# Optimization experiments

Measured on AMD Instinct MI355X. Metric: run time of the kernel, lower is better.

The kernel has to match this reference:

```python
import jax, jax.numpy as jnp
import numpy as np

H = 1024
V_IN = 32000
V_OUT = 32000
L = 256
START_ID = 1


def _gru_cell(x, h, Wi, Wh, bi, bh):
    # PyTorch GRU cell. x,h: [H]; Wi,Wh: [3H,H]; bi,bh: [3H]
    gi = Wi @ x + bi
    gh = Wh @ h + bh
    ir, iz, inn = jnp.split(gi, 3)
    hr, hz, hn = jnp.split(gh, 3)
    r = jax.nn.sigmoid(ir + hr)
    z = jax.nn.sigmoid(iz + hz)
    n = jnp.tanh(inn + r * hn)
    return (1.0 - z) * n + z * h


def setup_inputs() -> dict:
    key = jax.random.key(0)
    ks = jax.random.split(key, 20)
    s = 0.02
    d = {
        "input_ids": jax.random.randint(ks[0], (L,), 0, V_IN),
        "target_ids": jax.random.randint(ks[1], (L,), 0, V_OUT),
        "enc_emb": jax.random.normal(ks[2], (V_IN, H), jnp.float32) * s,
        "enc_Wi": jax.random.normal(ks[3], (3 * H, H), jnp.float32) * s,
        "enc_Wh": jax.random.normal(ks[4], (3 * H, H), jnp.float32) * s,
        "enc_bi": jnp.zeros((3 * H,), jnp.float32),
        "enc_bh": jnp.zeros((3 * H,), jnp.float32),
        "dec_emb": jax.random.normal(ks[5], (V_OUT, H), jnp.float32) * s,
        "dec_Wi": jax.random.normal(ks[6], (3 * H, H), jnp.float32) * s,
        "dec_Wh": jax.random.normal(ks[7], (3 * H, H), jnp.float32) * s,
        "dec_bi": jnp.zeros((3 * H,), jnp.float32),
        "dec_bh": jnp.zeros((3 * H,), jnp.float32),
        "attn_W": jax.random.normal(ks[8], (L, 2 * H), jnp.float32) * s,
        "attn_b": jnp.zeros((L,), jnp.float32),
        "comb_W": jax.random.normal(ks[9], (H, 2 * H), jnp.float32) * s,
        "comb_b": jnp.zeros((H,), jnp.float32),
        "out_W": jax.random.normal(ks[10], (V_OUT, H), jnp.float32) * s,
        "out_b": jnp.zeros((V_OUT,), jnp.float32),
    }
    return d


def reference(input_ids, target_ids, enc_emb, enc_Wi, enc_Wh, enc_bi, enc_bh,
              dec_emb, dec_Wi, dec_Wh, dec_bi, dec_bh,
              attn_W, attn_b, comb_W, comb_b, out_W, out_b):
    # ---- encoder: per-step GRU over input tokens, batch=1 ----
    enc_x = enc_emb[input_ids]  # [L, H]

    def enc_step(h, x):
        h2 = _gru_cell(x, h, enc_Wi, enc_Wh, enc_bi, enc_bh)
        return h2, h2

    h0 = jnp.zeros((H,), enc_emb.dtype)
    enc_hidden, enc_outs = jax.lax.scan(enc_step, h0, enc_x)  # enc_outs: [L, H]

    # ---- decoder with teacher forcing (deterministic branch) ----
    dec_in_ids = jnp.concatenate([jnp.array([START_ID], input_ids.dtype), target_ids[:-1]])

    def dec_step(h, inp):
        tok, tgt = inp
        e = dec_emb[tok]  # [H] (dropout in eval mode = identity)
        scores = attn_W @ jnp.concatenate([e, h]) + attn_b  # [L]
        a = jax.nn.softmax(scores)
        ctx = a @ enc_outs  # [H]
        c = jax.nn.relu(comb_W @ jnp.concatenate([e, ctx]) + comb_b)
        h2 = _gru_cell(c, h, dec_Wi, dec_Wh, dec_bi, dec_bh)
        logp = jax.nn.log_softmax(out_W @ h2 + out_b)  # [V_OUT]
        return h2, -logp[tgt]

    _, nll = jax.lax.scan(dec_step, enc_hidden, (dec_in_ids, target_ids))
    return jnp.sum(nll)
```

## Files before the change

kernel.cpp:

```cpp
#include <hip/hip_runtime.h>
#include <math.h>

#define H 1024
#define SEQ 256
#define VOUT 32000

typedef unsigned long long u64;

__device__ __forceinline__ float sigmoidf_(float x) { return 1.f / (1.f + expf(-x)); }

__device__ __forceinline__ u64 aload64(const u64* p) {
    return __hip_atomic_load(p, __ATOMIC_RELAXED, __HIP_MEMORY_SCOPE_AGENT);
}
__device__ __forceinline__ void publish(u64* p, float v, unsigned tag) {
    u64 pk = ((u64)tag << 32) | (u64)__float_as_uint(v);
    __hip_atomic_store(p, pk, __ATOMIC_RELAXED, __HIP_MEMORY_SCOPE_AGENT);
}
__device__ __forceinline__ float wait1(const u64* p, unsigned tag) {
    u64 v = aload64(p);
    while ((unsigned)(v >> 32) != tag) {
        __builtin_amdgcn_s_sleep(1);
        v = aload64(p);
    }
    return __uint_as_float((unsigned)v);
}
__device__ __forceinline__ void wait4(const u64* p0, const u64* p1,
                                      const u64* p2, const u64* p3, unsigned tag,
                                      float& o0, float& o1, float& o2, float& o3) {
    u64 v0 = aload64(p0), v1 = aload64(p1), v2 = aload64(p2), v3 = aload64(p3);
    while ((unsigned)(v0 >> 32) != tag || (unsigned)(v1 >> 32) != tag ||
           (unsigned)(v2 >> 32) != tag || (unsigned)(v3 >> 32) != tag) {
        __builtin_amdgcn_s_sleep(1);
        v0 = aload64(p0); v1 = aload64(p1); v2 = aload64(p2); v3 = aload64(p3);
    }
    o0 = __uint_as_float((unsigned)v0);
    o1 = __uint_as_float((unsigned)v1);
    o2 = __uint_as_float((unsigned)v2);
    o3 = __uint_as_float((unsigned)v3);
}

__global__ __launch_bounds__(256) void gather_kernel(
    const int* __restrict__ input_ids, const int* __restrict__ target_ids,
    const float* __restrict__ enc_emb, const float* __restrict__ dec_emb,
    float* __restrict__ enc_x, float* __restrict__ dec_e)
{
    int b = blockIdx.x, tid = threadIdx.x;
    if (b < SEQ) {
        int tok = input_ids[b];
        const float4* src = (const float4*)(enc_emb + (size_t)tok * H);
        float4* dst = (float4*)(enc_x + (size_t)b * H);
        dst[tid] = src[tid];
    } else {
        int t = b - SEQ;
        int tok = (t == 0) ? 1 : target_ids[t - 1];
        const float4* src = (const float4*)(dec_emb + (size_t)tok * H);
        float4* dst = (float4*)(dec_e + (size_t)t * H);
        dst[tid] = src[tid];
    }
}

__global__ __launch_bounds__(256) void init_kernel(u64* __restrict__ h64)
{
    int i = blockIdx.x * 256 + threadIdx.x;
    if (i < 2 * H) h64[i] = 0ULL;
}

__global__ __launch_bounds__(256) void gemm_nt_kernel(
    const float* __restrict__ A, const float* __restrict__ B,
    const float* __restrict__ bias, float* __restrict__ C,
    int Kdim, int lda, int offa, int ldb, int ldc)
{
    __shared__ float As[16][68];
    __shared__ float Bs[16][68];
    const int tid = threadIdx.x;
    const int m0 = blockIdx.y * 64;
    const int n0 = blockIdx.x * 64;
    const int tr = (tid >> 4) << 2;
    const int tc = (tid & 15) << 2;
    const int lrow = tid >> 2;
    const int lk = (tid & 3) << 2;
    const float* Ab = A + (size_t)m0 * lda + offa;
    const float* Bb = B + (size_t)n0 * ldb;
    float acc[4][4] = {{0.f,0.f,0.f,0.f},{0.f,0.f,0.f,0.f},{0.f,0.f,0.f,0.f},{0.f,0.f,0.f,0.f}};

    for (int k0 = 0; k0 < Kdim; k0 += 16) {
        float4 av = *(const float4*)(Ab + (size_t)lrow * lda + (k0 + lk));
        float4 bv = *(const float4*)(Bb + (size_t)lrow * ldb + (k0 + lk));
        As[lk + 0][lrow] = av.x; As[lk + 1][lrow] = av.y;
        As[lk + 2][lrow] = av.z; As[lk + 3][lrow] = av.w;
        Bs[lk + 0][lrow] = bv.x; Bs[lk + 1][lrow] = bv.y;
        Bs[lk + 2][lrow] = bv.z; Bs[lk + 3][lrow] = bv.w;
        __syncthreads();
#pragma unroll
        for (int k = 0; k < 16; ++k) {
            float4 a = *(const float4*)(&As[k][tr]);
            float4 b = *(const float4*)(&Bs[k][tc]);
            acc[0][0] = fmaf(a.x, b.x, acc[0][0]);
            acc[0][1] = fmaf(a.x, b.y, acc[0][1]);
            acc[0][2] = fmaf(a.x, b.z, acc[0][2]);
            acc[0][3] = fmaf(a.x, b.w, acc[0][3]);
            acc[1][0] = fmaf(a.y, b.x, acc[1][0]);
            acc[1][1] = fmaf(a.y, b.y, acc[1][1]);
            acc[1][2] = fmaf(a.y, b.z, acc[1][2]);
            acc[1][3] = fmaf(a.y, b.w, acc[1][3]);
            acc[2][0] = fmaf(a.z, b.x, acc[2][0]);
            acc[2][1] = fmaf(a.z, b.y, acc[2][1]);
            acc[2][2] = fmaf(a.z, b.z, acc[2][2]);
            acc[2][3] = fmaf(a.z, b.w, acc[2][3]);
            acc[3][0] = fmaf(a.w, b.x, acc[3][0]);
            acc[3][1] = fmaf(a.w, b.y, acc[3][1]);
            acc[3][2] = fmaf(a.w, b.z, acc[3][2]);
            acc[3][3] = fmaf(a.w, b.w, acc[3][3]);
        }
        __syncthreads();
    }
#pragma unroll
    for (int i = 0; i < 4; ++i) {
#pragma unroll
        for (int j = 0; j < 4; ++j) {
            float v = acc[i][j];
            if (bias) v += bias[n0 + tc + j];
            C[(size_t)(m0 + tr + i) * ldc + (n0 + tc + j)] = v;
        }
    }
}

__global__ __launch_bounds__(256, 1) void enc_rnn_kernel(
    const float* __restrict__ Wh, const float* __restrict__ bh,
    const float* __restrict__ gi_all,
    u64* __restrict__ h64, float* __restrict__ encH)
{
    __shared__ float h_s[2][H];
    const int tid = threadIdx.x;
    const int wave = tid >> 6, lane = tid & 63;
    const int u = blockIdx.x * 4 + wave;

    float rWr[16], rWz[16], rWn[16];
    {
        const float* wr = Wh + (size_t)u * H;
        const float* wz = Wh + (size_t)(u + H) * H;
        const float* wn = Wh + (size_t)(u + 2 * H) * H;
#pragma unroll
        for (int i = 0; i < 16; ++i) {
            int k = lane + (i << 6);
            rWr[i] = wr[k]; rWz[i] = wz[k]; rWn[i] = wn[k];
        }
    }
    const float bhr = bh[u], bhz = bh[H + u], bhn = bh[2 * H + u];

    for (int t = 0; t < SEQ; ++t) {
        const int p = t & 1;
        const float g0 = gi_all[t * 3 * H + u];
        const float g1 = gi_all[t * 3 * H + H + u];
        const float g2 = gi_all[t * 3 * H + 2 * H + u];

        u64* hs = h64 + p * H;
        float f0, f1, f2, f3;
        wait4(hs + tid, hs + tid + 256, hs + tid + 512, hs + tid + 768,
              (unsigned)t, f0, f1, f2, f3);
        h_s[p][tid]       = f0;
        h_s[p][tid + 256] = f1;
        h_s[p][tid + 512] = f2;
        h_s[p][tid + 768] = f3;
        __syncthreads();

        float dr = 0.f, dz = 0.f, dn = 0.f;
#pragma unroll
        for (int i = 0; i < 16; ++i) {
            float hv = h_s[p][lane + (i << 6)];
            dr = fmaf(rWr[i], hv, dr);
            dz = fmaf(rWz[i], hv, dz);
            dn = fmaf(rWn[i], hv, dn);
        }
#pragma unroll
        for (int off = 32; off > 0; off >>= 1) {
            dr += __shfl_down(dr, off);
            dz += __shfl_down(dz, off);
            dn += __shfl_down(dn, off);
        }
        if (lane == 0) {
            float r = sigmoidf_(g0 + dr + bhr);
            float z = sigmoidf_(g1 + dz + bhz);
            float n = tanhf(g2 + r * (dn + bhn));
            float h2 = (1.f - z) * n + z * h_s[p][u];
            publish(h64 + ((t + 1) & 1) * H + u, h2, (unsigned)(t + 1));
            encH[(size_t)t * H + u] = h2;
        }
    }
}

__global__ __launch_bounds__(256, 1) void dec_rnn_kernel(
    const float* __restrict__ attn_W, const float* __restrict__ attn_e,
    const float* __restrict__ M, const float* __restrict__ comb_pre,
    const float* __restrict__ Wi, const float* __restrict__ Wh,
    const float* __restrict__ bi, const float* __restrict__ bh,
    u64* __restrict__ h64, u64* __restrict__ s64,
    u64* __restrict__ c64, float* __restrict__ hs_dec)
{
    __shared__ float h_s[2][H];
    __shared__ float c_s[H];
    __shared__ float a_s[SEQ];
    __shared__ float red4[4];
    __shared__ float red4b[4];
    const int b = blockIdx.x, tid = threadIdx.x;
    const int wave = tid >> 6, lane = tid & 63;
    const int u = b * 4 + wave;

    float rWir[16], rWiz[16], rWin[16], rWhr[16], rWhz[16], rWhn[16];
    {
        const float* wir = Wi + (size_t)u * H;
        const float* wiz = Wi + (size_t)(u + H) * H;
        const float* win = Wi + (size_t)(u + 2 * H) * H;
        const float* whr = Wh + (size_t)u * H;
        const float* whz = Wh + (size_t)(u + H) * H;
        const float* whn = Wh + (size_t)(u + 2 * H) * H;
#pragma unroll
        for (int i = 0; i < 16; ++i) {
            int k = lane + (i << 6);
            rWir[i] = wir[k]; rWiz[i] = wiz[k]; rWin[i] = win[k];
            rWhr[i] = whr[k]; rWhz[i] = whz[k]; rWhn[i] = whn[k];
        }
    }
    float rA[4];
    {
        const float* arow = attn_W + (size_t)b * (2 * H) + H;
#pragma unroll
        for (int j = 0; j < 4; ++j) rA[j] = arow[tid + (j << 8)];
    }
    float rM[4];
    {
        const float* Mrow = M + (size_t)u * SEQ;
#pragma unroll
        for (int j = 0; j < 4; ++j) rM[j] = Mrow[lane + (j << 6)];
    }
    const float bir = bi[u], biz = bi[H + u], bin_ = bi[2 * H + u];
    const float bhr = bh[u], bhz = bh[H + u], bhn = bh[2 * H + u];

    for (int t = 0; t < SEQ; ++t) {
        const int p = t & 1;
        const unsigned htag = (unsigned)(SEQ + t);
        const unsigned stag = (unsigned)(t + 1);
        const float aev  = attn_e[t * SEQ + b];
        const float cpre = comb_pre[t * H + u];

        u64* hs = h64 + p * H;
        float hr0, hr1, hr2, hr3;
        wait4(hs + tid, hs + tid + 256, hs + tid + 512, hs + tid + 768,
              htag, hr0, hr1, hr2, hr3);
        h_s[p][tid]       = hr0;
        h_s[p][tid + 256] = hr1;
        h_s[p][tid + 512] = hr2;
        h_s[p][tid + 768] = hr3;

        float pp = fmaf(rA[0], hr0, 0.f);
        pp = fmaf(rA[1], hr1, pp);
        pp = fmaf(rA[2], hr2, pp);
        pp = fmaf(rA[3], hr3, pp);
#pragma unroll
        for (int off = 32; off > 0; off >>= 1) pp += __shfl_down(pp, off);
        if (lane == 0) red4[wave] = pp;
        __syncthreads();
        if (tid == 0)
            publish(s64 + b, red4[0] + red4[1] + red4[2] + red4[3] + aev, stag);

        float sv = wait1(s64 + tid, stag);
        float m = sv;
#pragma unroll
        for (int off = 32; off > 0; off >>= 1) m = fmaxf(m, __shfl_down(m, off));
        if (lane == 0) red4b[wave] = m;
        __syncthreads();
        float mx = fmaxf(fmaxf(red4b[0], red4b[1]), fmaxf(red4b[2], red4b[3]));
        float ev = expf(sv - mx);
        a_s[tid] = ev;
        float ssum = ev;
#pragma unroll
        for (int off = 32; off > 0; off >>= 1) ssum += __shfl_down(ssum, off);
        __syncthreads();
        if (lane == 0) red4b[wave] = ssum;
        __syncthreads();
        float inv = 1.f / (red4b[0] + red4b[1] + red4b[2] + red4b[3]);
        float pc = fmaf(a_s[lane], rM[0], 0.f);
        pc = fmaf(a_s[lane + 64],  rM[1], pc);
        pc = fmaf(a_s[lane + 128], rM[2], pc);
        pc = fmaf(a_s[lane + 192], rM[3], pc);
#pragma unroll
        for (int off = 32; off > 0; off >>= 1) pc += __shfl_down(pc, off);
        if (lane == 0)
            publish(c64 + u, fmaxf(0.f, cpre + pc * inv), stag);

        float c0, c1, c2, c3;
        wait4(c64 + tid, c64 + tid + 256, c64 + tid + 512, c64 + tid + 768,
              stag, c0, c1, c2, c3);
        c_s[tid]       = c0;
        c_s[tid + 256] = c1;
        c_s[tid + 512] = c2;
        c_s[tid + 768] = c3;
        __syncthreads();
        float dir = 0.f, diz = 0.f, din = 0.f, dhr = 0.f, dhz = 0.f, dhn = 0.f;
#pragma unroll
        for (int i = 0; i < 16; ++i) {
            int k = lane + (i << 6);
            float cv = c_s[k], hv = h_s[p][k];
            dir = fmaf(rWir[i], cv, dir);
            diz = fmaf(rWiz[i], cv, diz);
            din = fmaf(rWin[i], cv, din);
            dhr = fmaf(rWhr[i], hv, dhr);
            dhz = fmaf(rWhz[i], hv, dhz);
            dhn = fmaf(rWhn[i], hv, dhn);
        }
#pragma unroll
        for (int off = 32; off > 0; off >>= 1) {
            dir += __shfl_down(dir, off); diz += __shfl_down(diz, off);
            din += __shfl_down(din, off); dhr += __shfl_down(dhr, off);
            dhz += __shfl_down(dhz, off); dhn += __shfl_down(dhn, off);
        }
        if (lane == 0) {
            float r = sigmoidf_(dir + bir + dhr + bhr);
            float z = sigmoidf_(diz + biz + dhz + bhz);
            float n = tanhf(din + bin_ + r * (dhn + bhn));
            float h2 = (1.f - z) * n + z * h_s[p][u];
            publish(h64 + ((t + 1) & 1) * H + u, h2, htag + 1);
            hs_dec[(size_t)t * H + u] = h2;
        }
    }
}

__global__ __launch_bounds__(256) void nll_kernel(
    const float* __restrict__ logits, const int* __restrict__ target_ids,
    float* __restrict__ nll)
{
    const int t = blockIdx.x, tid = threadIdx.x;
    __shared__ float red[256];
    const float* row = logits + (size_t)t * VOUT;
    float mx = -1e30f;
    for (int i = tid; i < VOUT; i += 256) mx = fmaxf(mx, row[i]);
    red[tid] = mx;
    __syncthreads();
    for (int off = 128; off > 0; off >>= 1) {
        if (tid < off) red[tid] = fmaxf(red[tid], red[tid + off]);
        __syncthreads();
    }
    mx = red[0];
    __syncthreads();
    float s = 0.f;
    for (int i = tid; i < VOUT; i += 256) s += expf(row[i] - mx);
    red[tid] = s;
    __syncthreads();
    for (int off = 128; off > 0; off >>= 1) {
        if (tid < off) red[tid] += red[tid + off];
        __syncthreads();
    }
    if (tid == 0) {
        float lse = mx + logf(red[0]);
        nll[t] = lse - row[target_ids[t]];
    }
}

__global__ __launch_bounds__(256) void sum_kernel(
    const float* __restrict__ nll, float* __restrict__ out)
{
    __shared__ float red[256];
    int tid = threadIdx.x;
    red[tid] = nll[tid];
    __syncthreads();
    for (int off = 128; off > 0; off >>= 1) {
        if (tid < off) red[tid] += red[tid + off];
        __syncthreads();
    }
    if (tid == 0) out[0] = red[0];
}

extern "C" void kernel_launch(void* const* d_in, const int* in_sizes, int n_in,
                              void* d_out, int out_size, void* d_ws, size_t ws_size,
                              hipStream_t stream)
{
    const int*   input_ids  = (const int*)d_in[0];
    const int*   target_ids = (const int*)d_in[1];
    const float* enc_emb = (const float*)d_in[2];
    const float* enc_Wi  = (const float*)d_in[3];
    const float* enc_Wh  = (const float*)d_in[4];
    const float* enc_bi  = (const float*)d_in[5];
    const float* enc_bh  = (const float*)d_in[6];
    const float* dec_emb = (const float*)d_in[7];
    const float* dec_Wi  = (const float*)d_in[8];
    const float* dec_Wh  = (const float*)d_in[9];
    const float* dec_bi  = (const float*)d_in[10];
    const float* dec_bh  = (const float*)d_in[11];
    const float* attn_W  = (const float*)d_in[12];
    const float* attn_b  = (const float*)d_in[13];
    const float* comb_W  = (const float*)d_in[14];
    const float* comb_b  = (const float*)d_in[15];
    const float* out_W   = (const float*)d_in[16];
    const float* out_b   = (const float*)d_in[17];
    float* out = (float*)d_out;

    float* ws = (float*)d_ws;
    float* enc_x    = ws; ws += SEQ * H;
    float* dec_e    = ws; ws += SEQ * H;
    float* enc_gi   = ws; ws += SEQ * 3 * H;
    float* attn_e   = ws; ws += SEQ * SEQ;
    float* comb_pre = ws; ws += SEQ * H;
    float* Mmat     = ws; ws += H * SEQ;
    float* encH     = ws; ws += SEQ * H;
    float* hs_dec   = ws; ws += SEQ * H;
    u64*   h64      = (u64*)ws; ws += 2 * H * 2;
    u64*   s64      = (u64*)ws; ws += SEQ * 2;
    u64*   c64      = (u64*)ws; ws += H * 2;
    float* nll      = ws; ws += SEQ;
    ws += (256 - ((ws - (float*)d_ws) & 255)) & 255;
    float* logits   = ws; ws += (size_t)SEQ * VOUT;

    hipLaunchKernelGGL(gather_kernel, dim3(512), dim3(256), 0, stream,
                       input_ids, target_ids, enc_emb, dec_emb, enc_x, dec_e);
    hipLaunchKernelGGL(init_kernel, dim3(8), dim3(256), 0, stream, h64);

    hipLaunchKernelGGL(gemm_nt_kernel, dim3(3 * H / 64, SEQ / 64), dim3(256), 0, stream,
                       enc_x, enc_Wi, enc_bi, enc_gi, H, H, 0, H, 3 * H);
    hipLaunchKernelGGL(gemm_nt_kernel, dim3(SEQ / 64, SEQ / 64), dim3(256), 0, stream,
                       dec_e, attn_W, attn_b, attn_e, H, H, 0, 2 * H, SEQ);
    hipLaunchKernelGGL(gemm_nt_kernel, dim3(H / 64, SEQ / 64), dim3(256), 0, stream,
                       dec_e, comb_W, comb_b, comb_pre, H, H, 0, 2 * H, H);

    {
        void* args[] = {(void*)&enc_Wh, (void*)&enc_bh, (void*)&enc_gi,
                        (void*)&h64, (void*)&encH};
        hipLaunchCooperativeKernel((void*)enc_rnn_kernel, dim3(256), dim3(256),
                                   args, 0, stream);
    }

    hipLaunchKernelGGL(gemm_nt_kernel, dim3(SEQ / 64, H / 64), dim3(256), 0, stream,
                       comb_W, encH, (const float*)nullptr, Mmat, H, 2 * H, H, H, SEQ);

    {
        void* args[] = {(void*)&attn_W, (void*)&attn_e, (void*)&Mmat, (void*)&comb_pre,
                        (void*)&dec_Wi, (void*)&dec_Wh, (void*)&dec_bi, (void*)&dec_bh,
                        (void*)&h64, (void*)&s64, (void*)&c64, (void*)&hs_dec};
        hipLaunchCooperativeKernel((void*)dec_rnn_kernel, dim3(256), dim3(256),
                                   args, 0, stream);
    }

    hipLaunchKernelGGL(gemm_nt_kernel, dim3(VOUT / 64, SEQ / 64), dim3(256), 0, stream,
                       hs_dec, out_W, out_b, logits, H, H, 0, H, VOUT);

    hipLaunchKernelGGL(nll_kernel, dim3(SEQ), dim3(256), 0, stream,
                       logits, target_ids, nll);
    hipLaunchKernelGGL(sum_kernel, dim3(1), dim3(256), 0, stream, nll, out);
}
```

Measured before the change: 4.688 ms.

## Use sentinel-gated cohort polling in RNN kernels and enlarge GEMM tile to 128x64

Before each cross-block exchange, a few threads first spin on sentinel slots (the last entry of each 256-chunk). All threads then poll their own values once, and a block-wide __syncthreads_and decides whether to retry. The goal is to cut global polling traffic from every thread spinning on its own slots. Separately, the NT GEMM tile grows from 64x64 to 128x64 with 8x4 accumulators per thread, raising arithmetic intensity per shared-memory load but halving the grid size for the small GEMMs. The sentinel check assumes the last-written slot implies the others are ready, and the cohort loop keeps a retry as a fallback, so it should stay correct either way.

New measurement: 4.321 ms. -7.8%, faster.

```diff
diff --git a/kernel.cpp b/kernel.cpp
--- a/kernel.cpp
+++ b/kernel.cpp
@@ -16,27 +16,35 @@
     u64 pk = ((u64)tag << 32) | (u64)__float_as_uint(v);
     __hip_atomic_store(p, pk, __ATOMIC_RELAXED, __HIP_MEMORY_SCOPE_AGENT);
 }
-__device__ __forceinline__ float wait1(const u64* p, unsigned tag) {
-    u64 v = aload64(p);
-    while ((unsigned)(v >> 32) != tag) {
-        __builtin_amdgcn_s_sleep(1);
-        v = aload64(p);
-    }
-    return __uint_as_float((unsigned)v);
-}
-__device__ __forceinline__ void wait4(const u64* p0, const u64* p1,
-                                      const u64* p2, const u64* p3, unsigned tag,
-                                      float& o0, float& o1, float& o2, float& o3) {
-    u64 v0 = aload64(p0), v1 = aload64(p1), v2 = aload64(p2), v3 = aload64(p3);
-    while ((unsigned)(v0 >> 32) != tag || (unsigned)(v1 >> 32) != tag ||
-           (unsigned)(v2 >> 32) != tag || (unsigned)(v3 >> 32) != tag) {
-        __builtin_amdgcn_s_sleep(1);
-        v0 = aload64(p0); v1 = aload64(p1); v2 = aload64(p2); v3 = aload64(p3);
-    }
-    o0 = __uint_as_float((unsigned)v0);
-    o1 = __uint_as_float((unsigned)v1);
-    o2 = __uint_as_float((unsigned)v2);
-    o3 = __uint_as_float((unsigned)v3);
+__device__ __forceinline__ void waittag(const u64* p, unsigned tag) {
+    while ((unsigned)(aload64(p) >> 32) != tag) __builtin_amdgcn_s_sleep(1);
+}
+__device__ __forceinline__ void cohort_pull4(
+    const u64* p0, const u64* p1, const u64* p2, const u64* p3, unsigned tag,
+    float& o0, float& o1, float& o2, float& o3)
+{
+    for (;;) {
+        u64 v0 = aload64(p0), v1 = aload64(p1), v2 = aload64(p2), v3 = aload64(p3);
+        int ok = ((unsigned)(v0 >> 32) == tag) & ((unsigned)(v1 >> 32) == tag) &
+                 ((unsigned)(v2 >> 32) == tag) & ((unsigned)(v3 >> 32) == tag);
+        if (__syncthreads_and(ok)) {
+            o0 = __uint_as_float((unsigned)v0);
+            o1 = __uint_as_float((unsigned)v1);
+            o2 = __uint_as_float((unsigned)v2);
+            o3 = __uint_as_float((unsigned)v3);
+            return;
+        }
+        __builtin_amdgcn_s_sleep(2);
+    }
+}
+__device__ __forceinline__ float cohort_pull1(const u64* p, unsigned tag)
+{
+    for (;;) {
+        u64 v = aload64(p);
+        int ok = ((unsigned)(v >> 32) == tag);
+        if (__syncthreads_and(ok)) return __uint_as_float((unsigned)v);
+        __builtin_amdgcn_s_sleep(2);
+    }
 }
 
 __global__ __launch_bounds__(256) void gather_kernel(
@@ -70,52 +78,51 @@
     const float* __restrict__ bias, float* __restrict__ C,
     int Kdim, int lda, int offa, int ldb, int ldc)
 {
-    __shared__ float As[16][68];
+    __shared__ float As[16][136];
     __shared__ float Bs[16][68];
     const int tid = threadIdx.x;
-    const int m0 = blockIdx.y * 64;
+    const int m0 = blockIdx.y * 128;
     const int n0 = blockIdx.x * 64;
-    const int tr = (tid >> 4) << 2;
+    const int tr = (tid >> 4) << 3;
     const int tc = (tid & 15) << 2;
     const int lrow = tid >> 2;
     const int lk = (tid & 3) << 2;
     const float* Ab = A + (size_t)m0 * lda + offa;
     const float* Bb = B + (size_t)n0 * ldb;
-    float acc[4][4] = {{0.f,0.f,0.f,0.f},{0.f,0.f,0.f,0.f},{0.f,0.f,0.f,0.f},{0.f,0.f,0.f,0.f}};
+    float acc[8][4];
+#pragma unroll
+    for (int i = 0; i < 8; ++i)
+#pragma unroll
+        for (int j = 0; j < 4; ++j) acc[i][j] = 0.f;
 
     for (int k0 = 0; k0 < Kdim; k0 += 16) {
-        float4 av = *(const float4*)(Ab + (size_t)lrow * lda + (k0 + lk));
+        float4 a0 = *(const float4*)(Ab + (size_t)lrow * lda + (k0 + lk));
+        float4 a1 = *(const float4*)(Ab + (size_t)(lrow + 64) * lda + (k0 + lk));
         float4 bv = *(const float4*)(Bb + (size_t)lrow * ldb + (k0 + lk));
-        As[lk + 0][lrow] = av.x; As[lk + 1][lrow] = av.y;
-        As[lk + 2][lrow] = av.z; As[lk + 3][lrow] = av.w;
+        As[lk + 0][lrow] = a0.x; As[lk + 1][lrow] = a0.y;
+        As[lk + 2][lrow] = a0.z; As[lk + 3][lrow] = a0.w;
+        As[lk + 0][lrow + 64] = a1.x; As[lk + 1][lrow + 64] = a1.y;
+        As[lk + 2][lrow + 64] = a1.z; As[lk + 3][lrow + 64] = a1.w;
         Bs[lk + 0][lrow] = bv.x; Bs[lk + 1][lrow] = bv.y;
         Bs[lk + 2][lrow] = bv.z; Bs[lk + 3][lrow] = bv.w;
         __syncthreads();
 #pragma unroll
         for (int k = 0; k < 16; ++k) {
-            float4 a = *(const float4*)(&As[k][tr]);
-            float4 b = *(const float4*)(&Bs[k][tc]);
-            acc[0][0] = fmaf(a.x, b.x, acc[0][0]);
-            acc[0][1] = fmaf(a.x, b.y, acc[0][1]);
-            acc[0][2] = fmaf(a.x, b.z, acc[0][2]);
-            acc[0][3] = fmaf(a.x, b.w, acc[0][3]);
-            acc[1][0] = fmaf(a.y, b.x, acc[1][0]);
-            acc[1][1] = fmaf(a.y, b.y, acc[1][1]);
-            acc[1][2] = fmaf(a.y, b.z, acc[1][2]);
-            acc[1][3] = fmaf(a.y, b.w, acc[1][3]);
-            acc[2][0] = fmaf(a.z, b.x, acc[2][0]);
-            acc[2][1] = fmaf(a.z, b.y, acc[2][1]);
-            acc[2][2] = fmaf(a.z, b.z, acc[2][2]);
-            acc[2][3] = fmaf(a.z, b.w, acc[2][3]);
-            acc[3][0] = fmaf(a.w, b.x, acc[3][0]);
-            acc[3][1] = fmaf(a.w, b.y, acc[3][1]);
-            acc[3][2] = fmaf(a.w, b.z, acc[3][2]);
-            acc[3][3] = fmaf(a.w, b.w, acc[3][3]);
-        }
-        __syncthreads();
-    }
-#pragma unroll
-    for (int i = 0; i < 4; ++i) {
+            float4 aA = *(const float4*)(&As[k][tr]);
+            float4 aB = *(const float4*)(&As[k][tr + 4]);
+            float4 b  = *(const float4*)(&Bs[k][tc]);
+            float a8[8] = {aA.x, aA.y, aA.z, aA.w, aB.x, aB.y, aB.z, aB.w};
+            float b4[4] = {b.x, b.y, b.z, b.w};
+#pragma unroll
+            for (int i = 0; i < 8; ++i)
+#pragma unroll
+                for (int j = 0; j < 4; ++j)
+                    acc[i][j] = fmaf(a8[i], b4[j], acc[i][j]);
+        }
+        __syncthreads();
+    }
+#pragma unroll
+    for (int i = 0; i < 8; ++i) {
 #pragma unroll
         for (int j = 0; j < 4; ++j) {
             float v = acc[i][j];
@@ -155,9 +162,11 @@
         const float g2 = gi_all[t * 3 * H + 2 * H + u];
 
         u64* hs = h64 + p * H;
+        if (tid < 4) waittag(hs + 255 + (tid << 8), (unsigned)t);
+        __syncthreads();
         float f0, f1, f2, f3;
-        wait4(hs + tid, hs + tid + 256, hs + tid + 512, hs + tid + 768,
-              (unsigned)t, f0, f1, f2, f3);
+        cohort_pull4(hs + tid, hs + tid + 256, hs + tid + 512, hs + tid + 768,
+                     (unsigned)t, f0, f1, f2, f3);
         h_s[p][tid]       = f0;
         h_s[p][tid + 256] = f1;
         h_s[p][tid + 512] = f2;
@@ -244,9 +253,11 @@
         const float cpre = comb_pre[t * H + u];
 
         u64* hs = h64 + p * H;
+        if (tid < 4) waittag(hs + 255 + (tid << 8), htag);
+        __syncthreads();
         float hr0, hr1, hr2, hr3;
-        wait4(hs + tid, hs + tid + 256, hs + tid + 512, hs + tid + 768,
-              htag, hr0, hr1, hr2, hr3);
+        cohort_pull4(hs + tid, hs + tid + 256, hs + tid + 512, hs + tid + 768,
+                     htag, hr0, hr1, hr2, hr3);
         h_s[p][tid]       = hr0;
         h_s[p][tid + 256] = hr1;
         h_s[p][tid + 512] = hr2;
@@ -263,7 +274,9 @@
         if (tid == 0)
             publish(s64 + b, red4[0] + red4[1] + red4[2] + red4[3] + aev, stag);
 
-        float sv = wait1(s64 + tid, stag);
+        if (tid == 0) waittag(s64 + 255, stag);
+        __syncthreads();
+        float sv = cohort_pull1(s64 + tid, stag);
         float m = sv;
 #pragma unroll
         for (int off = 32; off > 0; off >>= 1) m = fmaxf(m, __shfl_down(m, off));
@@ -288,9 +301,11 @@
         if (lane == 0)
             publish(c64 + u, fmaxf(0.f, cpre + pc * inv), stag);
 
+        if (tid < 4) waittag(c64 + 255 + (tid << 8), stag);
+        __syncthreads();
         float c0, c1, c2, c3;
-        wait4(c64 + tid, c64 + tid + 256, c64 + tid + 512, c64 + tid + 768,
-              stag, c0, c1, c2, c3);
+        cohort_pull4(c64 + tid, c64 + tid + 256, c64 + tid + 512, c64 + tid + 768,
+                     stag, c0, c1, c2, c3);
         c_s[tid]       = c0;
         c_s[tid + 256] = c1;
         c_s[tid + 512] = c2;
@@ -414,11 +429,11 @@
                        input_ids, target_ids, enc_emb, dec_emb, enc_x, dec_e);
     hipLaunchKernelGGL(init_kernel, dim3(8), dim3(256), 0, stream, h64);
 
-    hipLaunchKernelGGL(gemm_nt_kernel, dim3(3 * H / 64, SEQ / 64), dim3(256), 0, stream,
+    hipLaunchKernelGGL(gemm_nt_kernel, dim3(3 * H / 64, SEQ / 128), dim3(256), 0, stream,
                        enc_x, enc_Wi, enc_bi, enc_gi, H, H, 0, H, 3 * H);
-    hipLaunchKernelGGL(gemm_nt_kernel, dim3(SEQ / 64, SEQ / 64), dim3(256), 0, stream,
+    hipLaunchKernelGGL(gemm_nt_kernel, dim3(SEQ / 64, SEQ / 128), dim3(256), 0, stream,
                        dec_e, attn_W, attn_b, attn_e, H, H, 0, 2 * H, SEQ);
-    hipLaunchKernelGGL(gemm_nt_kernel, dim3(H / 64, SEQ / 64), dim3(256), 0, stream,
+    hipLaunchKernelGGL(gemm_nt_kernel, dim3(H / 64, SEQ / 128), dim3(256), 0, stream,
                        dec_e, comb_W, comb_b, comb_pre, H, H, 0, 2 * H, H);
 
     {
@@ -428,7 +443,7 @@
                                    args, 0, stream);
     }
 
-    hipLaunchKernelGGL(gemm_nt_kernel, dim3(SEQ / 64, H / 64), dim3(256), 0, stream,
+    hipLaunchKernelGGL(gemm_nt_kernel, dim3(SEQ / 64, H / 128), dim3(256), 0, stream,
                        comb_W, encH, (const float*)nullptr, Mmat, H, 2 * H, H, H, SEQ);
 
     {
@@ -439,7 +454,7 @@
                                    args, 0, stream);
     }
 
-    hipLaunchKernelGGL(gemm_nt_kernel, dim3(VOUT / 64, SEQ / 64), dim3(256), 0, stream,
+    hipLaunchKernelGGL(gemm_nt_kernel, dim3(VOUT / 64, SEQ / 128), dim3(256), 0, stream,
                        hs_dec, out_W, out_b, logits, H, H, 0, H, VOUT);
 
     hipLaunchKernelGGL(nll_kernel, dim3(SEQ), dim3(256), 0, stream,
```
